# Optimization experiments

Hardware: AMD Instinct MI355X
Metric: run time of the kernel (lower is better)

## Reference

```python
import jax, jax.numpy as jnp
import numpy as np

D_MODEL = 1024
N_HEADS = 16
HEAD_DIM = D_MODEL // N_HEADS


def setup_inputs() -> dict:
    key = jax.random.key(0)
    ks = jax.random.split(key, 9)
    s = 1.0 / np.sqrt(D_MODEL)
    return {
        "x": jax.random.normal(ks[0], (4, 2048, D_MODEL), dtype=jnp.float32),
        "Wq": jax.random.normal(ks[1], (D_MODEL, D_MODEL), dtype=jnp.float32) * s,
        "bq": jax.random.normal(ks[2], (D_MODEL,), dtype=jnp.float32) * 0.01,
        "Wk": jax.random.normal(ks[3], (D_MODEL, D_MODEL), dtype=jnp.float32) * s,
        "bk": jax.random.normal(ks[4], (D_MODEL,), dtype=jnp.float32) * 0.01,
        "Wv": jax.random.normal(ks[5], (D_MODEL, D_MODEL), dtype=jnp.float32) * s,
        "bv": jax.random.normal(ks[6], (D_MODEL,), dtype=jnp.float32) * 0.01,
        "Wo": jax.random.normal(ks[7], (D_MODEL, D_MODEL), dtype=jnp.float32) * s,
        "bo": jax.random.normal(ks[8], (D_MODEL,), dtype=jnp.float32) * 0.01,
    }


def reference(x, Wq, bq, Wk, bk, Wv, bv, Wo, bo):
    b, s, d = x.shape  # [batch, seq, d_model]
    # projections (weights stored as [d_in, d_out], equiv to torch Linear W.T)
    q = x @ Wq + bq
    k = x @ Wk + bk
    v = x @ Wv + bv
    # split heads -> [b, h, s, hd]
    q = q.reshape(b, s, N_HEADS, HEAD_DIM).transpose(0, 2, 1, 3)
    k = k.reshape(b, s, N_HEADS, HEAD_DIM).transpose(0, 2, 1, 3)
    v = v.reshape(b, s, N_HEADS, HEAD_DIM).transpose(0, 2, 1, 3)
    scale = 1.0 / jnp.sqrt(jnp.asarray(HEAD_DIM, dtype=q.dtype))
    scores = jnp.einsum("bhqd,bhkd->bhqk", q, k) * scale  # [b,h,s,s]
    attn = jax.nn.softmax(scores, axis=-1)
    y = jnp.einsum("bhqk,bhkd->bhqd", attn, v)
    y = y.transpose(0, 2, 1, 3).reshape(b, s, d)
    return y @ Wo + bo
```

## Files before the change

### kernel.cpp

```cpp
#include <hip/hip_runtime.h>

#define SEQ   2048
#define DM    1024
#define NH    16
#define HD    64
#define MTOT  8192
#define QSCALE 0.18033688011112042f
#define SMAX  12.0f

typedef _Float16 f16x8 __attribute__((ext_vector_type(8)));
typedef float    f32x4 __attribute__((ext_vector_type(4)));

__device__ __forceinline__ unsigned short f2h(float f) {
    _Float16 h = (_Float16)f;
    return __builtin_bit_cast(unsigned short, h);
}
__device__ __forceinline__ float h2f(unsigned short u) {
    return (float)__builtin_bit_cast(_Float16, u);
}
__device__ __forceinline__ unsigned int pkrtz(float a, float b) {
    return __builtin_bit_cast(unsigned int, __builtin_amdgcn_cvt_pkrtz(a, b));
}
__device__ __forceinline__ float fexp2(float x) {
    return __builtin_amdgcn_exp2f(x);
}
__device__ __forceinline__ void async_cp16(const void* g, void* l) {
    __builtin_amdgcn_global_load_lds(
        (const __attribute__((address_space(1))) unsigned int*)g,
        (__attribute__((address_space(3))) unsigned int*)l, 16, 0, 0);
}

__global__ __launch_bounds__(256) void convert_x_kernel(
    const float* __restrict__ x, unsigned short* __restrict__ Xh)
{
    const size_t i8 = ((size_t)blockIdx.x * 256 + threadIdx.x) * 8;
    float f[8];
    *(float4*)&f[0] = *(const float4*)(x + i8);
    *(float4*)&f[4] = *(const float4*)(x + i8 + 4);
    unsigned short h[8];
#pragma unroll
    for (int e = 0; e < 8; ++e) h[e] = f2h(f[e]);
    uint4 ph;
    ph.x = h[0] | ((unsigned)h[1] << 16); ph.y = h[2] | ((unsigned)h[3] << 16);
    ph.z = h[4] | ((unsigned)h[5] << 16); ph.w = h[6] | ((unsigned)h[7] << 16);
    *(uint4*)(Xh + i8) = ph;
}

__global__ __launch_bounds__(256) void convert_w_kernel(
    const float* __restrict__ Wq, const float* __restrict__ Wk,
    const float* __restrict__ Wv, const float* __restrict__ Wo,
    unsigned short* __restrict__ WTh, unsigned short* __restrict__ WTl)
{
    __shared__ float tile[32][33];
    const int z = blockIdx.z;
    const float* W = (z == 0) ? Wq : (z == 1) ? Wk : (z == 2) ? Wv : Wo;
    const float s = (z == 0) ? QSCALE : 1.0f;
    const int r0 = blockIdx.y << 5, c0 = blockIdx.x << 5;
    const int tx = threadIdx.x, ty = threadIdx.y;
#pragma unroll
    for (int u = 0; u < 4; ++u)
        tile[ty + 8 * u][tx] = W[(size_t)(r0 + ty + 8 * u) * DM + c0 + tx];
    __syncthreads();
#pragma unroll
    for (int u = 0; u < 4; ++u) {
        const int dout = c0 + ty + 8 * u;
        const int din  = r0 + tx;
        const float v = tile[tx][ty + 8 * u] * s;
        const unsigned short hh = f2h(v);
        const size_t idx = (size_t)(z * DM + dout) * DM + din;
        WTh[idx] = hh;
        if (z == 3) WTl[idx] = f2h(v - h2f(hh));
    }
}

__global__ __launch_bounds__(512, 2) void qkv_kernel(
    const unsigned short* __restrict__ Ag,
    const unsigned short* __restrict__ Bg,
    const float* __restrict__ b0, const float* __restrict__ b1,
    const float* __restrict__ b2,
    unsigned short* __restrict__ Qf, unsigned short* __restrict__ Kf,
    unsigned short* __restrict__ Vt)
{
    extern __shared__ unsigned short gsm[];

    const int t = threadIdx.x;
    const int wave = t >> 6, L = t & 63;
    const int quad = L >> 4, l16 = L & 15;
    const int xk = l16 & 7;
    const int wr = wave >> 2, wc = wave & 3;
    const int m0 = blockIdx.x << 8;
    const int n0 = blockIdx.y << 7;

    const int srow = L >> 3;
    const int sck  = (L & 7) ^ srow;

    f32x4 acc[8][2] = {};

    #define STAGE_A(buf, half, k0)                                              \
        _Pragma("unroll")                                                       \
        for (int u = 0; u < 2; ++u)                                             \
            async_cp16(Ag + (size_t)(m0 + (half)*128 + wave*16 + u*8 + srow) * DM \
                          + (k0) + sck*8,                                       \
                       &gsm[(buf)*16384 + (half)*8192 + wave*1024 + u*512]);
    #define STAGE_B(buf, k0)                                                    \
        _Pragma("unroll")                                                       \
        for (int u = 0; u < 2; ++u)                                             \
            async_cp16(Bg + (size_t)(n0 + wave*16 + u*8 + srow) * DM            \
                          + (k0) + sck*8,                                       \
                       &gsm[32768 + (buf)*8192 + wave*1024 + u*512]);

    STAGE_A(0, 0, 0);
    STAGE_A(0, 1, 0);
    STAGE_B(0, 0);
    __syncthreads();

    for (int tk = 0; tk < 16; ++tk) {
        const int cur = tk & 1, nxt = cur ^ 1;
        const int k1 = (tk + 1) << 6;
        const int abase = cur * 16384 + wr * 8192;
        const int bbase = 32768 + cur * 8192;

        if (tk < 15) {
            STAGE_A(nxt, 0, k1);
            STAGE_B(nxt, k1);
        }
        f16x8 fb[2][2];
#pragma unroll
        for (int j = 0; j < 2; ++j)
#pragma unroll
            for (int ks = 0; ks < 2; ++ks)
                fb[j][ks] = *(const f16x8*)&gsm[bbase
                    + ((wc << 5) + (j << 4) + l16) * 64
                    + ((((ks << 2) + quad) ^ xk) << 3)];
        {
            f16x8 fa[4][2];
#pragma unroll
            for (int i = 0; i < 4; ++i)
#pragma unroll
                for (int ks = 0; ks < 2; ++ks)
                    fa[i][ks] = *(const f16x8*)&gsm[abase
                        + ((i << 4) + l16) * 64
                        + ((((ks << 2) + quad) ^ xk) << 3)];
            __builtin_amdgcn_s_barrier();
            __builtin_amdgcn_s_setprio(1);
#pragma unroll
            for (int i = 0; i < 4; ++i)
#pragma unroll
                for (int j = 0; j < 2; ++j)
#pragma unroll
                    for (int ks = 0; ks < 2; ++ks)
                        acc[i][j] = __builtin_amdgcn_mfma_f32_16x16x32_f16(
                            fa[i][ks], fb[j][ks], acc[i][j], 0, 0, 0);
            __builtin_amdgcn_s_setprio(0);
            __builtin_amdgcn_s_barrier();
        }

        if (tk < 15) {
            STAGE_A(nxt, 1, k1);
        }
        {
            f16x8 fa[4][2];
#pragma unroll
            for (int i = 0; i < 4; ++i)
#pragma unroll
                for (int ks = 0; ks < 2; ++ks)
                    fa[i][ks] = *(const f16x8*)&gsm[abase
                        + ((64 + (i << 4) + l16)) * 64
                        + ((((ks << 2) + quad) ^ xk) << 3)];
            __builtin_amdgcn_s_barrier();
            __builtin_amdgcn_s_setprio(1);
#pragma unroll
            for (int i = 0; i < 4; ++i)
#pragma unroll
                for (int j = 0; j < 2; ++j)
#pragma unroll
                    for (int ks = 0; ks < 2; ++ks)
                        acc[4 + i][j] = __builtin_amdgcn_mfma_f32_16x16x32_f16(
                            fa[i][ks], fb[j][ks], acc[4 + i][j], 0, 0, 0);
            __builtin_amdgcn_s_setprio(0);
        }

        __syncthreads();
    }
    #undef STAGE_A
    #undef STAGE_B

#pragma unroll
    for (int j = 0; j < 2; ++j) {
        const int col = n0 + (wc << 5) + (j << 4) + l16;
        const int seg = col >> 10;
        const int c = col & 1023;
        const int h_ = c >> 6, d_ = c & 63;
        const float bj = (seg == 0) ? b0[c] * QSCALE : (seg == 1) ? b1[c] : b2[c];
        unsigned short* Op = (seg == 0) ? Qf : Kf;
#pragma unroll
        for (int i8 = 0; i8 < 8; ++i8) {
            const int row0 = m0 + (wr << 7) + (i8 << 4) + (quad << 2);
            const int b_ = row0 >> 11, s0 = row0 & 2047;
            if (seg < 2) {
                const size_t ib = ((size_t)b_ * NH + h_) * SEQ;
#pragma unroll
                for (int r = 0; r < 4; ++r)
                    Op[(ib + s0 + r) * HD + d_] = f2h(acc[i8][j][r] + bj);
            } else {
                unsigned short e[4];
#pragma unroll
                for (int r = 0; r < 4; ++r) e[r] = f2h(acc[i8][j][r] + bj);
                const size_t idx = (((size_t)b_ * NH + h_) * HD + d_) * SEQ + s0;
                uint2 pv;
                pv.x = e[0] | ((unsigned)e[1] << 16);
                pv.y = e[2] | ((unsigned)e[3] << 16);
                *(uint2*)&Vt[idx] = pv;
            }
        }
    }
}

__global__ __launch_bounds__(256, 3) void gemm_kernel(
    const unsigned short* __restrict__ Agh, const unsigned short* __restrict__ Agl,
    const unsigned short* __restrict__ Bgh, const unsigned short* __restrict__ Bgl,
    const float* __restrict__ b0,
    float* __restrict__ Cf)
{
    __shared__ unsigned short gsm[16384];

    const int t = threadIdx.x;
    const int wave = t >> 6, L = t & 63;
    const int quad = L >> 4, l16 = L & 15;
    const int m0 = blockIdx.x << 7, n0 = blockIdx.y << 7;

    const int trl = L >> 2;
    const int ck  = (L & 3) ^ (trl & 3);
    const unsigned short* gsrc = (wave == 0) ? Agh : (wave == 1) ? Agl
                               : (wave == 2) ? Bgh : Bgl;
    const int rbase = (wave < 2) ? m0 : n0;
    const unsigned short* gl = gsrc + (size_t)(rbase + trl) * DM + ck * 8;
    unsigned short* lb = &gsm[wave << 12];

    const int wm = (wave >> 1) << 6, wn = (wave & 1) << 6;
    const int xk2 = l16 & 3;
    f32x4 acc[4][4] = {};

    for (int k0 = 0; k0 < DM; k0 += 32) {
        __syncthreads();
#pragma unroll
        for (int u = 0; u < 8; ++u)
            async_cp16(gl + (size_t)u * 16 * DM + k0, lb + (u << 9));
        __syncthreads();

        f16x8 fah[4], fal[4], fbh[4], fbl[4];
#pragma unroll
        for (int i = 0; i < 4; ++i) {
            const int ao = (wm + (i << 4) + l16) * 32 + ((quad ^ xk2) << 3);
            fah[i] = *(const f16x8*)&gsm[ao];
            fal[i] = *(const f16x8*)&gsm[4096 + ao];
        }
#pragma unroll
        for (int j = 0; j < 4; ++j) {
            const int bo_ = (wn + (j << 4) + l16) * 32 + ((quad ^ xk2) << 3);
            fbh[j] = *(const f16x8*)&gsm[8192 + bo_];
            fbl[j] = *(const f16x8*)&gsm[12288 + bo_];
        }
#pragma unroll
        for (int i = 0; i < 4; ++i)
#pragma unroll
            for (int j = 0; j < 4; ++j) {
                acc[i][j] = __builtin_amdgcn_mfma_f32_16x16x32_f16(fah[i], fbh[j], acc[i][j], 0, 0, 0);
                acc[i][j] = __builtin_amdgcn_mfma_f32_16x16x32_f16(fal[i], fbh[j], acc[i][j], 0, 0, 0);
                acc[i][j] = __builtin_amdgcn_mfma_f32_16x16x32_f16(fah[i], fbl[j], acc[i][j], 0, 0, 0);
            }
    }

#pragma unroll
    for (int j = 0; j < 4; ++j) {
        const int col = n0 + wn + (j << 4) + l16;
        const float bj = b0[col];
#pragma unroll
        for (int i = 0; i < 4; ++i)
#pragma unroll
            for (int r = 0; r < 4; ++r) {
                const int row = m0 + wm + (i << 4) + (quad << 2) + r;
                Cf[(size_t)row * DM + col] = acc[i][j][r] + bj;
            }
    }
}

__global__ __launch_bounds__(256, 4) void attn_kernel(
    const unsigned short* __restrict__ Qg,
    const unsigned short* __restrict__ Kg,
    const unsigned short* __restrict__ Vg,
    unsigned short* __restrict__ Yh, unsigned short* __restrict__ Yl)
{
    __shared__ unsigned short smem[20480];

    const int t = threadIdx.x;
    const int wave = t >> 6, L = t & 63;
    const int quad = L >> 4, l16 = L & 15;
    const int xk = l16 & 7;
    const int bh = blockIdx.x;
    const int q0 = blockIdx.y << 7;
    const size_t base = (size_t)bh * SEQ * HD;

    f16x8 fQ[2][2];
#pragma unroll
    for (int nt = 0; nt < 2; ++nt) {
        const size_t qr = (size_t)(q0 + (wave << 5) + (nt << 4) + l16);
#pragma unroll
        for (int ks = 0; ks < 2; ++ks)
            fQ[nt][ks] = *(const f16x8*)(Qg + base + qr * HD + (ks << 5) + (quad << 3));
    }

    const int trl = L >> 3;
    const int sck = (L & 7) ^ trl;
    const unsigned short* sg = (wave == 0) ? Kg : Vg;
    const size_t rstr = (wave == 1) ? (size_t)SEQ : (size_t)HD;
    const unsigned short* gbase = sg + base + trl * rstr + sck * 8;

    float lsum[2] = {0.0f, 0.0f};
    f32x4 o[2][4] = {};
    f32x4 sacc[2][4];

    auto STAGE = [&](int kt) {
        if (wave < 2) {
            const size_t koff = (wave == 0) ? ((size_t)kt << 12) : ((size_t)kt << 6);
            unsigned short* lb = (wave == 0) ? smem
                                             : &smem[4096 + ((kt & 1) << 12)];
            const unsigned short* g = gbase + koff;
#pragma unroll
            for (int u = 0; u < 8; ++u)
                async_cp16(g + ((size_t)u << 3) * rstr, lb + (u << 9));
        }
    };
    auto QK = [&]() {
#pragma unroll
        for (int nt = 0; nt < 2; ++nt)
#pragma unroll
            for (int mt = 0; mt < 4; ++mt)
                sacc[nt][mt] = (f32x4){-SMAX, -SMAX, -SMAX, -SMAX};
        __builtin_amdgcn_s_setprio(1);
#pragma unroll
        for (int mt = 0; mt < 4; ++mt) {
#pragma unroll
            for (int ks = 0; ks < 2; ++ks) {
                const int off = ((mt << 4) + l16) * 64 + ((((ks << 2) + quad) ^ xk) << 3);
                const f16x8 fK = *(const f16x8*)&smem[off];
#pragma unroll
                for (int nt = 0; nt < 2; ++nt)
                    sacc[nt][mt] = __builtin_amdgcn_mfma_f32_16x16x32_f16(fK, fQ[nt][ks], sacc[nt][mt], 0, 0, 0);
            }
        }
        __builtin_amdgcn_s_setprio(0);
    };
    auto SMPV = [&](int ktp) {
        const int vb = 4096 + ((ktp & 1) << 12);
#pragma unroll
        for (int nt = 0; nt < 2; ++nt) {
            const int prow = (wave << 5) + (nt << 4) + l16;
#pragma unroll
            for (int mt = 0; mt < 4; ++mt) {
                float p[4];
#pragma unroll
                for (int r = 0; r < 4; ++r) {
                    p[r] = fexp2(sacc[nt][mt][r]);
                    lsum[nt] += p[r];
                }
                uint2 pk;
                pk.x = pkrtz(p[0], p[1]);
                pk.y = pkrtz(p[2], p[3]);
                const int ch = ((mt << 1) + (quad >> 1)) ^ xk;
                *(uint2*)&smem[12288 + prow * 64 + (ch << 3) + ((quad & 1) << 2)] = pk;
            }
        }
        f16x8 fV[4][2];
#pragma unroll
        for (int dt = 0; dt < 4; ++dt)
#pragma unroll
            for (int ks = 0; ks < 2; ++ks) {
                const int off = vb + ((dt << 4) + l16) * 64 + ((((ks << 2) + quad) ^ xk) << 3);
                fV[dt][ks] = *(const f16x8*)&smem[off];
            }
#pragma unroll
        for (int nt = 0; nt < 2; ++nt) {
            const int prow = (wave << 5) + (nt << 4) + l16;
            f16x8 fP[2];
#pragma unroll
            for (int ks = 0; ks < 2; ++ks) {
                const int off = 12288 + prow * 64 + ((((ks << 2) + quad) ^ xk) << 3);
                fP[ks] = *(const f16x8*)&smem[off];
            }
            __builtin_amdgcn_s_setprio(1);
#pragma unroll
            for (int dt = 0; dt < 4; ++dt)
#pragma unroll
                for (int ks = 0; ks < 2; ++ks)
                    o[nt][dt] = __builtin_amdgcn_mfma_f32_16x16x32_f16(fP[ks], fV[dt][ks], o[nt][dt], 0, 0, 0);
            __builtin_amdgcn_s_setprio(0);
        }
    };

    STAGE(0);
    __syncthreads();
    QK();

    for (int kt = 1; kt < 32; ++kt) {
        __syncthreads();
        STAGE(kt);
        SMPV(kt - 1);
        __syncthreads();
        QK();
    }
    SMPV(31);

#pragma unroll
    for (int nt = 0; nt < 2; ++nt) {
        lsum[nt] += __shfl_xor(lsum[nt], 16);
        lsum[nt] += __shfl_xor(lsum[nt], 32);
    }
    const int b_ = bh >> 4, h_ = bh & 15;
#pragma unroll
    for (int nt = 0; nt < 2; ++nt) {
        const float linv = 1.0f / lsum[nt];
        float lr[4];
#pragma unroll
        for (int r = 0; r < 4; ++r) lr[r] = __shfl(linv, (quad << 2) + r);
#pragma unroll
        for (int dt = 0; dt < 4; ++dt)
#pragma unroll
            for (int r = 0; r < 4; ++r) {
                const int row = q0 + (wave << 5) + (nt << 4) + (quad << 2) + r;
                const float v = o[nt][dt][r] * lr[r];
                const size_t idx = ((size_t)b_ * SEQ + row) * DM + (h_ << 6) + (dt << 4) + l16;
                const unsigned short hh = f2h(v);
                Yh[idx] = hh;
                Yl[idx] = f2h(v - h2f(hh));
            }
    }
}

extern "C" void kernel_launch(void* const* d_in, const int* in_sizes, int n_in,
                              void* d_out, int out_size, void* d_ws, size_t ws_size,
                              hipStream_t stream)
{
    const float* x  = (const float*)d_in[0];
    const float* Wq = (const float*)d_in[1];
    const float* bq = (const float*)d_in[2];
    const float* Wk = (const float*)d_in[3];
    const float* bk = (const float*)d_in[4];
    const float* Wv = (const float*)d_in[5];
    const float* bv = (const float*)d_in[6];
    const float* Wo = (const float*)d_in[7];
    const float* bo = (const float*)d_in[8];
    float* out = (float*)d_out;

    char* w = (char*)d_ws;
    unsigned short* Xh  = (unsigned short*)(w);
    unsigned short* Yl  = (unsigned short*)(w + (16u << 20));
    unsigned short* Qf  = (unsigned short*)(w + (32u << 20));
    unsigned short* Kf  = (unsigned short*)(w + (48u << 20));
    unsigned short* Vt  = (unsigned short*)(w + (64u << 20));
    unsigned short* WTh = (unsigned short*)(w + (112u << 20));
    unsigned short* WTl = (unsigned short*)(w + (120u << 20));
    unsigned short* Yh = Xh;

    hipFuncSetAttribute(reinterpret_cast<const void*>(qkv_kernel),
                        hipFuncAttributeMaxDynamicSharedMemorySize, 98304);

    convert_x_kernel<<<dim3(MTOT * DM / (256 * 8)), dim3(256), 0, stream>>>(x, Xh);
    convert_w_kernel<<<dim3(32, 32, 4), dim3(32, 8), 0, stream>>>(Wq, Wk, Wv, Wo, WTh, WTl);

    qkv_kernel<<<dim3(32, 24), dim3(512), 98304, stream>>>(
        Xh, WTh, bq, bk, bv, Qf, Kf, Vt);

    attn_kernel<<<dim3(4 * NH, SEQ / 128), dim3(256), 0, stream>>>(
        Qf, Kf, Vt, Yh, Yl);

    gemm_kernel<<<dim3(64, 8), dim3(256), 0, stream>>>(
        Yh, Yl, WTh + (size_t)3072 * DM, WTl + (size_t)3072 * DM,
        bo, out);
}
```

Baseline: 298.7 us.

## Triple-buffer QKV GEMM shared-memory tiles with two-stage async prefetch

The QKV projection GEMM moves from double to triple buffering in shared memory. Tiles are prefetched two k-steps ahead, and the per-step __syncthreads plus mid-step barriers are replaced by a vmcnt wait and a single barrier per iteration. This is meant to hide global-load latency better and cut synchronisation. In exchange, dynamic LDS grows to 144KB per block, which limits occupancy to one block per CU. The counted-wait logic must match the number of outstanding copies exactly.

```diff
diff --git a/kernel.cpp b/kernel.cpp
--- a/kernel.cpp
+++ b/kernel.cpp
@@ -107,23 +107,27 @@
         for (int u = 0; u < 2; ++u)                                             \
             async_cp16(Bg + (size_t)(n0 + wave*16 + u*8 + srow) * DM            \
                           + (k0) + sck*8,                                       \
-                       &gsm[32768 + (buf)*8192 + wave*1024 + u*512]);
-
-    STAGE_A(0, 0, 0);
-    STAGE_A(0, 1, 0);
-    STAGE_B(0, 0);
-    __syncthreads();
+                       &gsm[49152 + (buf)*8192 + wave*1024 + u*512]);
+
+    STAGE_A(0, 0, 0);  STAGE_A(0, 1, 0);  STAGE_B(0, 0);
+    STAGE_A(1, 0, 64); STAGE_A(1, 1, 64); STAGE_B(1, 64);
+    asm volatile("s_waitcnt vmcnt(6)" ::: "memory");
+    __builtin_amdgcn_s_barrier();
 
     for (int tk = 0; tk < 16; ++tk) {
-        const int cur = tk & 1, nxt = cur ^ 1;
-        const int k1 = (tk + 1) << 6;
-        const int abase = cur * 16384 + wr * 8192;
-        const int bbase = 32768 + cur * 8192;
-
-        if (tk < 15) {
-            STAGE_A(nxt, 0, k1);
-            STAGE_B(nxt, k1);
-        }
+        const int buf  = tk % 3;
+        const int nbuf = (tk + 2) % 3;
+        const int k2   = (tk + 2) << 6;
+
+        if (tk < 14) {
+            STAGE_A(nbuf, 0, k2);
+            STAGE_A(nbuf, 1, k2);
+            STAGE_B(nbuf, k2);
+        }
+
+        const int abase = buf * 16384 + wr * 8192;
+        const int bbase = 49152 + buf * 8192;
+
         f16x8 fb[2][2];
 #pragma unroll
         for (int j = 0; j < 2; ++j)
@@ -152,12 +156,8 @@
                         acc[i][j] = __builtin_amdgcn_mfma_f32_16x16x32_f16(
                             fa[i][ks], fb[j][ks], acc[i][j], 0, 0, 0);
             __builtin_amdgcn_s_setprio(0);
-            __builtin_amdgcn_s_barrier();
-        }
-
-        if (tk < 15) {
-            STAGE_A(nxt, 1, k1);
-        }
+        }
+
         {
             f16x8 fa[4][2];
 #pragma unroll
@@ -167,7 +167,6 @@
                     fa[i][ks] = *(const f16x8*)&gsm[abase
                         + ((64 + (i << 4) + l16)) * 64
                         + ((((ks << 2) + quad) ^ xk) << 3)];
-            __builtin_amdgcn_s_barrier();
             __builtin_amdgcn_s_setprio(1);
 #pragma unroll
             for (int i = 0; i < 4; ++i)
@@ -180,7 +179,12 @@
             __builtin_amdgcn_s_setprio(0);
         }
 
-        __syncthreads();
+        if (tk < 14)
+            asm volatile("s_waitcnt vmcnt(6)" ::: "memory");
+        else if (tk == 14)
+            asm volatile("s_waitcnt vmcnt(0)" ::: "memory");
+        if (tk < 15)
+            __builtin_amdgcn_s_barrier();
     }
     #undef STAGE_A
     #undef STAGE_B
@@ -463,12 +467,12 @@
     unsigned short* Yh = Xh;
 
     hipFuncSetAttribute(reinterpret_cast<const void*>(qkv_kernel),
-                        hipFuncAttributeMaxDynamicSharedMemorySize, 98304);
+                        hipFuncAttributeMaxDynamicSharedMemorySize, 147456);
 
     convert_x_kernel<<<dim3(MTOT * DM / (256 * 8)), dim3(256), 0, stream>>>(x, Xh);
     convert_w_kernel<<<dim3(32, 32, 4), dim3(32, 8), 0, stream>>>(Wq, Wk, Wv, Wo, WTh, WTl);
 
-    qkv_kernel<<<dim3(32, 24), dim3(512), 98304, stream>>>(
+    qkv_kernel<<<dim3(32, 24), dim3(512), 147456, stream>>>(
         Xh, WTh, bq, bk, bv, Qf, Kf, Vt);
 
     attn_kernel<<<dim3(4 * NH, SEQ / 128), dim3(256), 0, stream>>>(
```

Result: no change. 302.0 us (+1.1%).
